# Performance work log

Measured on AMD Instinct MI355X. Metric: run time of the kernel, lower is better.

The kernel has to match this reference:

```python
import jax, jax.numpy as jnp
import numpy as np

WS = 8      # window size
SS = 4      # shift size
NH = 4      # num heads
EPS = 1e-5
MLP_RATIO = 4


def _win_part(x, ws):
    # x: [B,D,H,W,C] -> [B*nD*nH*nW, ws^3, C]
    B, D, H, W, C = x.shape
    x = x.reshape(B, D // ws, ws, H // ws, ws, W // ws, ws, C)
    x = x.transpose(0, 1, 3, 5, 2, 4, 6, 7)
    return x.reshape(-1, ws * ws * ws, C)


def _win_rev(w, ws, B, D, H, W):
    C = w.shape[-1]
    x = w.reshape(B, D // ws, H // ws, W // ws, ws, ws, ws, C)
    x = x.transpose(0, 1, 4, 2, 5, 3, 6, 7)
    return x.reshape(B, D, H, W, C)


def _ln(x, g, b):
    m = jnp.mean(x, axis=-1, keepdims=True)
    v = jnp.mean((x - m) ** 2, axis=-1, keepdims=True)
    return (x - m) / jnp.sqrt(v + EPS) * g + b


def _rel_index(ws):
    coords = np.stack(np.meshgrid(np.arange(ws), np.arange(ws), np.arange(ws), indexing='ij'))  # [3,ws,ws,ws]
    cf = coords.reshape(3, -1)                      # [3, ws^3]
    rel = (cf[:, :, None] - cf[:, None, :]).transpose(1, 2, 0) + (ws - 1)  # [N,N,3]
    return rel[..., 0] * (2 * ws - 1) ** 2 + rel[..., 1] * (2 * ws - 1) + rel[..., 2]


def _attn_mask(D, H, W, ws, ss):
    img = np.zeros((1, D, H, W, 1), dtype=np.float32)
    cnt = 0
    sl = (slice(0, -ws), slice(-ws, -ss), slice(-ss, None))
    for d in sl:
        for h in sl:
            for w in sl:
                img[:, d, h, w, :] = cnt
                cnt += 1
    mw = np.asarray(_win_part(jnp.asarray(img), ws))[..., 0]  # [nW, ws^3]
    diff = mw[:, None, :] - mw[:, :, None]
    return np.where(diff != 0, -100.0, 0.0).astype(np.float32)


def setup_inputs() -> dict:
    key = jax.random.key(0)
    ks = jax.random.split(key, 12)
    B, D, H, W, C = 1, 16, 64, 64, 128
    mh = MLP_RATIO * C
    s = 0.02
    return {
        'x': jax.random.normal(ks[0], (B, D, H, W, C), jnp.float32),
        'attn_mask': jnp.asarray(_attn_mask(D, H, W, WS, SS)),
        'rel_index': jnp.asarray(_rel_index(WS), jnp.int32),
        'rel_bias': jax.random.normal(ks[1], ((2 * WS - 1) ** 3, NH), jnp.float32) * s,
        'qkv_w': jax.random.normal(ks[2], (3 * C, C), jnp.float32) * s,
        'qkv_b': jnp.zeros((3 * C,), jnp.float32),
        'proj_w': jax.random.normal(ks[3], (C, C), jnp.float32) * s,
        'proj_b': jnp.zeros((C,), jnp.float32),
        'norm1_g': jnp.ones((C,), jnp.float32),
        'norm1_b': jnp.zeros((C,), jnp.float32),
        'norm2_g': jnp.ones((C,), jnp.float32),
        'norm2_b': jnp.zeros((C,), jnp.float32),
        'mlp_w1': jax.random.normal(ks[4], (mh, C), jnp.float32) * s,
        'mlp_b1': jnp.zeros((mh,), jnp.float32),
        'mlp_w2': jax.random.normal(ks[5], (C, mh), jnp.float32) * s,
        'mlp_b2': jnp.zeros((C,), jnp.float32),
    }


def reference(x, attn_mask, rel_index, rel_bias, qkv_w, qkv_b, proj_w, proj_b,
              norm1_g, norm1_b, norm2_g, norm2_b, mlp_w1, mlp_b1, mlp_w2, mlp_b2):
    B, D, H, W, C = x.shape
    ws, ss, nh = WS, SS, NH
    hd = C // nh
    scale = hd ** -0.5
    N = ws ** 3
    shortcut = x
    h = _ln(x, norm1_g, norm1_b)
    h = jnp.roll(h, (-ss, -ss, -ss), axis=(1, 2, 3))
    xw = _win_part(h, ws)                 # [B_, N, C]
    B_ = xw.shape[0]
    nW = attn_mask.shape[0]
    qkv = xw @ qkv_w.T + qkv_b            # [B_, N, 3C]
    qkv = qkv.reshape(B_, N, 3, nh, hd).transpose(2, 0, 3, 1, 4)  # [3,B_,h,N,hd]
    q, k, v = qkv[0] * scale, qkv[1], qkv[2]
    attn = jnp.einsum('bhnd,bhmd->bhnm', q, k)
    rpe = rel_bias[rel_index.reshape(-1)].reshape(N, N, nh).transpose(2, 0, 1)  # [h,N,N]
    attn = attn + rpe[None]
    attn = attn.reshape(B_ // nW, nW, nh, N, N) + attn_mask[None, :, None]
    attn = jax.nn.softmax(attn.reshape(B_, nh, N, N), axis=-1)
    out = jnp.einsum('bhnm,bhmd->bhnd', attn, v).transpose(0, 2, 1, 3).reshape(B_, N, C)
    out = out @ proj_w.T + proj_b
    out = _win_rev(out, ws, B, D, H, W)
    out = jnp.roll(out, (ss, ss, ss), axis=(1, 2, 3))
    x = shortcut + out
    h2 = _ln(x, norm2_g, norm2_b)
    h2 = jax.nn.gelu(h2 @ mlp_w1.T + mlp_b1, approximate=False)
    return x + h2 @ mlp_w2.T + mlp_b2
```

## Files before the change

kernel.cpp:

```cpp
#include <hip/hip_runtime.h>
#include <math.h>

typedef __bf16 bf16;
typedef __bf16 bf16x4 __attribute__((ext_vector_type(4)));
typedef __bf16 bf16x8 __attribute__((ext_vector_type(8)));
typedef float f32x4 __attribute__((ext_vector_type(4)));
typedef unsigned short u16;
typedef u16 u16x2 __attribute__((ext_vector_type(2)));

#define LOG2E 1.4426950408889634f

__device__ __forceinline__ float b2f(u16 b) {
  return (float)__builtin_bit_cast(bf16, b);
}

__global__ void sniff_k(const unsigned* __restrict__ xw_, int* __restrict__ flag) {
  int lane = threadIdx.x;
  int c = 0;
#pragma unroll
  for (int j = 0; j < 4; j++) {
    unsigned e = (xw_[lane * 4 + j] >> 7) & 0xFFu;
    c += (e >= 100u && e <= 140u) ? 1 : 0;
  }
#pragma unroll
  for (int d = 1; d < 64; d <<= 1) c += __shfl_xor(c, d);
  if (lane == 0) *flag = (c >= 150) ? 1 : 0;
}

struct ProArgs {
  const int* ridx;
  const void* rbias;
  bf16* rpem;
  const void* x;
  const bf16* g1;
  const bf16* b1n;
  bf16* xw;
  const void* csrc[12];
  bf16* cdst[12];
  int cn[12];
};

__global__ __launch_bounds__(256) void pro_k(ProArgs a,
                                             const int* __restrict__ flag) {
  const int bx = blockIdx.x, tid = threadIdx.x;
  const int fl = *flag;
  if (bx < 8192) {
    int t = bx * 256 + tid;
    int m0 = (t & 127) * 4, q = (t >> 7) & 511, h = (t >> 16) & 3, ty = t >> 18;
    int qd = q >> 6, qh = (q >> 3) & 7, qw = q & 7;
    int kt = m0 >> 6, mt = (m0 >> 4) & 3, quad = (m0 >> 2) & 3;
    int4 ri = *(const int4*)&a.ridx[q * 512 + m0];
    const int rv[4] = {ri.x, ri.y, ri.z, ri.w};
    bf16x4 o;
#pragma unroll
    for (int j = 0; j < 4; j++) {
      int m = m0 + j;
      int md = m >> 6, mh = (m >> 3) & 7, mw = m & 7;
      bool diff = ((ty & 4) && ((qd < 4) != (md < 4))) ||
                  ((ty & 2) && ((qh < 4) != (mh < 4))) ||
                  ((ty & 1) && ((qw < 4) != (mw < 4)));
      float bv = fl ? (float)((const bf16*)a.rbias)[rv[j] * 4 + h]
                    : ((const float*)a.rbias)[rv[j] * 4 + h];
      float v = bv * LOG2E;
      o[j] = (bf16)(v + (diff ? -144.2695041f : 0.f));
    }
    size_t out = ((size_t)(ty * 4 + h) << 18) +
                 (((size_t)(kt * 4 + quad) * 512 + q) * 16 + mt * 4);
    *(bf16x4*)&a.rpem[out] = o;
  } else if (bx < 24576) {
    int wave = tid >> 6, lane = tid & 63;
    int tok = (bx - 8192) * 4 + wave;
    int win = tok >> 9, pos = tok & 511;
    int rd = (win >> 6) * 8 + (pos >> 6);
    int rh = ((win >> 3) & 7) * 8 + ((pos >> 3) & 7);
    int rw = (win & 7) * 8 + (pos & 7);
    int od = (rd + 4) & 15, oh = (rh + 4) & 63, ow = (rw + 4) & 63;
    size_t src = (size_t)((od * 64 + oh) * 64 + ow) * 128;
    int ch = lane * 2;
    float f0, f1;
    if (!fl) {
      const float* xf = (const float*)a.x + src + ch;
      f0 = xf[0];
      f1 = xf[1];
    } else {
      u16x2 xv = *(const u16x2*)((const bf16*)a.x + src + ch);
      f0 = b2f(xv[0]);
      f1 = b2f(xv[1]);
    }
    float s = f0 + f1, sq = f0 * f0 + f1 * f1;
#pragma unroll
    for (int d = 1; d < 64; d <<= 1) {
      s += __shfl_xor(s, d);
      sq += __shfl_xor(sq, d);
    }
    float mean = s * (1.f / 128.f);
    float var = sq * (1.f / 128.f) - mean * mean;
    float rstd = rsqrtf(fmaxf(var, 0.f) + 1e-5f);
    u16x2 gv = *(const u16x2*)(a.g1 + ch), bv = *(const u16x2*)(a.b1n + ch);
    u16x2 ov;
    ov[0] =
        __builtin_bit_cast(u16, (bf16)((f0 - mean) * rstd * b2f(gv[0]) + b2f(bv[0])));
    ov[1] =
        __builtin_bit_cast(u16, (bf16)((f1 - mean) * rstd * b2f(gv[1]) + b2f(bv[1])));
    *(u16x2*)(a.xw + (size_t)tok * 128 + ch) = ov;
  } else {
    int seg = bx - 24576;
    int ti = seg >> 8;
    int i = (seg & 255) * 256 + tid;
    if (i < a.cn[ti]) {
      if (fl)
        a.cdst[ti][i] = ((const bf16*)a.csrc[ti])[i];
      else
        a.cdst[ti][i] = (bf16)((const float*)a.csrc[ti])[i];
    }
  }
}

__global__ __launch_bounds__(256) void ln_k(const bf16* __restrict__ x,
                                            const bf16* __restrict__ g,
                                            const bf16* __restrict__ bsh,
                                            bf16* __restrict__ out) {
  int wave = threadIdx.x >> 6, lane = threadIdx.x & 63;
  int tok = blockIdx.x * 4 + wave;
  size_t src = (size_t)tok * 128;
  int ch = lane * 2;
  u16x2 xv = *(const u16x2*)(x + src + ch);
  float f0 = b2f(xv[0]), f1 = b2f(xv[1]);
  float s = f0 + f1, sq = f0 * f0 + f1 * f1;
#pragma unroll
  for (int d = 1; d < 64; d <<= 1) {
    s += __shfl_xor(s, d);
    sq += __shfl_xor(sq, d);
  }
  float mean = s * (1.f / 128.f);
  float var = sq * (1.f / 128.f) - mean * mean;
  float rstd = rsqrtf(fmaxf(var, 0.f) + 1e-5f);
  u16x2 gv = *(const u16x2*)(g + ch), bv = *(const u16x2*)(bsh + ch);
  u16x2 ov;
  ov[0] = __builtin_bit_cast(u16, (bf16)((f0 - mean) * rstd * b2f(gv[0]) + b2f(bv[0])));
  ov[1] = __builtin_bit_cast(u16, (bf16)((f1 - mean) * rstd * b2f(gv[1]) + b2f(bv[1])));
  *(u16x2*)(out + (size_t)tok * 128 + ch) = ov;
}

template <int EPI, int BM, int BK, int N_, int K_>
__global__ __launch_bounds__(256) void gemm_k(const bf16* __restrict__ A,
                                              const bf16* __restrict__ B,
                                              const bf16* __restrict__ bias,
                                              void* __restrict__ outv,
                                              const void* __restrict__ residv,
                                              const int* __restrict__ flag) {
  constexpr int NC = K_ / BK;
  constexpr int NBUF = (NC > 1) ? 2 : 1;
  __shared__ __align__(16) u16 SM[NBUF][(BM + 128) * BK];
  const int t = threadIdx.x;
  const int wave = t >> 6, lane = t & 63, l15 = lane & 15, quad = lane >> 4;
  const int m0 = blockIdx.x * BM, n0 = blockIdx.y * 128;
  constexpr int MI = BM / 32;
  int fl = 0;
  if constexpr (EPI == 1) fl = *flag;
  f32x4 acc[MI][4] = {};
  const int wr = (wave >> 1) * (BM / 2), wc = (wave & 1) * 64;
  constexpr int TPR = BK / 8;
  constexpr int RPP = 256 / TPR;
  constexpr int PASSES = (BM + 128) / RPP;
  const int srow = t / TPR, sc16 = t % TPR;

  auto stage = [&](int c, int buf) {
#pragma unroll
    for (int p = 0; p < PASSES; p++) {
      int row = p * RPP + srow;
      int cs = sc16 ^ (row & 7);
      const u16* src;
      if (row < BM)
        src = (const u16*)A + (size_t)(m0 + row) * K_ + c * BK + cs * 8;
      else
        src = (const u16*)B + (size_t)(n0 + row - BM) * K_ + c * BK + cs * 8;
      __builtin_amdgcn_global_load_lds(
          (const __attribute__((address_space(1))) void*)src,
          (__attribute__((address_space(3))) void*)&SM[buf][row * BK + sc16 * 8],
          16, 0, 0);
    }
  };

  stage(0, 0);
  __syncthreads();
#pragma unroll
  for (int c = 0; c < NC; c++) {
    if (c + 1 < NC) stage(c + 1, (c + 1) & 1);
    const char* cur = (const char*)SM[c & 1];
#pragma unroll
    for (int ks = 0; ks < BK / 32; ks++) {
      bf16x8 a[MI], b[4];
#pragma unroll
      for (int i = 0; i < MI; i++) {
        int row = wr + i * 16 + l15;
        a[i] = *(const bf16x8*)(cur + row * (BK * 2) +
                                (((ks * 4 + quad) ^ (row & 7)) << 4));
      }
#pragma unroll
      for (int j = 0; j < 4; j++) {
        int row = BM + wc + j * 16 + l15;
        b[j] = *(const bf16x8*)(cur + row * (BK * 2) +
                                (((ks * 4 + quad) ^ (row & 7)) << 4));
      }
#pragma unroll
      for (int i = 0; i < MI; i++)
#pragma unroll
        for (int j = 0; j < 4; j++)
          acc[i][j] =
              __builtin_amdgcn_mfma_f32_16x16x32_bf16(a[i], b[j], acc[i][j], 0, 0, 0);
    }
    if (c + 1 < NC) __syncthreads();
  }
  const float qscale = 0.17677669529663687f * LOG2E;
#pragma unroll
  for (int i = 0; i < MI; i++) {
#pragma unroll
    for (int r = 0; r < 4; r++) {
      int tok = m0 + wr + i * 16 + quad * 4 + r;
      size_t obase = 0;
      if constexpr (EPI == 1) {
        int win = tok >> 9, pos = tok & 511;
        int rd = (win >> 6) * 8 + (pos >> 6);
        int rh = ((win >> 3) & 7) * 8 + ((pos >> 3) & 7);
        int rw = (win & 7) * 8 + (pos & 7);
        int od = (rd + 4) & 15, oh = (rh + 4) & 63, ow = (rw + 4) & 63;
        obase = (size_t)((od * 64 + oh) * 64 + ow) * 128;
      }
#pragma unroll
      for (int j = 0; j < 4; j++) {
        int gn = n0 + wc + j * 16 + l15;
        float v = acc[i][j][r] + (float)bias[gn];
        if constexpr (EPI == 0) {
          int tensor = gn >> 7, c = gn & 127, head = c >> 5, d = c & 31;
          if (tensor == 0) v *= qscale;
          int win = tok >> 9, pos = tok & 511;
          size_t off = ((((size_t)tensor * 4 + head) * 128 + win) * 512 + pos) * 32 + d;
          ((bf16*)outv)[off] = (bf16)v;
        } else {
          float rs = fl ? (float)((const bf16*)residv)[obase + gn]
                        : ((const float*)residv)[obase + gn];
          v += rs;
          ((bf16*)outv)[obase + gn] = (bf16)v;
        }
      }
    }
  }
}

__global__ __launch_bounds__(256) void mlp_k(const bf16* __restrict__ A,
                                             const bf16* __restrict__ W1,
                                             const bf16* __restrict__ B1,
                                             const bf16* __restrict__ W2,
                                             const bf16* __restrict__ B2,
                                             const bf16* __restrict__ resid,
                                             void* __restrict__ outv,
                                             const int* __restrict__ flag) {
  __shared__ __align__(16) u16 sA[32 * 128];
  __shared__ __align__(16) u16 sB[128 * 128];
  __shared__ __align__(16) u16 sH[32 * 520];
  const int t = threadIdx.x;
  const int wave = t >> 6, lane = t & 63, l15 = lane & 15, quad = lane >> 4;
  const int m0 = blockIdx.x * 32;
  const int wr = (wave >> 1) * 16, wc = (wave & 1) * 64;
  const int fl = *flag;
  const int srow = t >> 4, sc16 = t & 15;

  auto stage_w = [&](const bf16* W, int chunk, int wK) {
#pragma unroll
    for (int p = 0; p < 8; p++) {
      int row = p * 16 + srow;
      int cs = sc16 ^ (row & 7);
      const u16* src = (const u16*)W + (size_t)(wK == 128 ? (chunk * 128 + row) : row) *
                                           wK +
                       (wK == 128 ? 0 : chunk * 128) + cs * 8;
      __builtin_amdgcn_global_load_lds(
          (const __attribute__((address_space(1))) void*)src,
          (__attribute__((address_space(3))) void*)&sB[row * 128 + sc16 * 8], 16,
          0, 0);
    }
  };

  {
#pragma unroll
    for (int p = 0; p < 2; p++) {
      int row = p * 16 + srow;
      int cs = sc16 ^ (row & 7);
      __builtin_amdgcn_global_load_lds(
          (const __attribute__((address_space(1))) void*)((const u16*)A +
                                                          (size_t)(m0 + row) * 128 +
                                                          cs * 8),
          (__attribute__((address_space(3))) void*)&sA[row * 128 + sc16 * 8], 16,
          0, 0);
    }
  }
  stage_w(W1, 0, 128);
  __syncthreads();

#pragma unroll 1
  for (int nc = 0; nc < 4; nc++) {
    f32x4 acc1[4] = {};
#pragma unroll
    for (int ks = 0; ks < 4; ks++) {
      int arow = wr + l15;
      bf16x8 av = *(const bf16x8*)((const char*)sA + arow * 256 +
                                   (((ks * 4 + quad) ^ (arow & 7)) << 4));
      bf16x8 bv[4];
#pragma unroll
      for (int j = 0; j < 4; j++) {
        int row = wc + j * 16 + l15;
        bv[j] = *(const bf16x8*)((const char*)sB + row * 256 +
                                 (((ks * 4 + quad) ^ (row & 7)) << 4));
      }
#pragma unroll
      for (int j = 0; j < 4; j++)
        acc1[j] = __builtin_amdgcn_mfma_f32_16x16x32_bf16(av, bv[j], acc1[j], 0, 0, 0);
    }
#pragma unroll
    for (int j = 0; j < 4; j++) {
      int ncol = nc * 128 + wc + j * 16 + l15;
      float bj = (float)B1[ncol];
#pragma unroll
      for (int r = 0; r < 4; r++) {
        float v = acc1[j][r] + bj;
        float v2 = v * v;
        float u2 = v * (2.30220806f + 0.10294323f * v2);
        float e2 = exp2f(u2);
        v = v - v * __builtin_amdgcn_rcpf(e2 + 1.f);
        sH[(wr + quad * 4 + r) * 520 + ncol] = __builtin_bit_cast(u16, (bf16)v);
      }
    }
    __syncthreads();
    if (nc < 3)
      stage_w(W1, nc + 1, 128);
    else
      stage_w(W2, 0, 512);
    __syncthreads();
  }

  f32x4 acc2[4] = {};
#pragma unroll 1
  for (int kc = 0; kc < 4; kc++) {
#pragma unroll
    for (int ks = 0; ks < 4; ks++) {
      int arow = wr + l15;
      bf16x8 av = *(const bf16x8*)((const char*)sH + arow * 1040 +
                                   (kc * 128 + ks * 32 + quad * 8) * 2);
      bf16x8 bv[4];
#pragma unroll
      for (int j = 0; j < 4; j++) {
        int row = wc + j * 16 + l15;
        bv[j] = *(const bf16x8*)((const char*)sB + row * 256 +
                                 (((ks * 4 + quad) ^ (row & 7)) << 4));
      }
#pragma unroll
      for (int j = 0; j < 4; j++)
        acc2[j] = __builtin_amdgcn_mfma_f32_16x16x32_bf16(av, bv[j], acc2[j], 0, 0, 0);
    }
    if (kc < 3) {
      __syncthreads();
      stage_w(W2, kc + 1, 512);
      __syncthreads();
    }
  }
#pragma unroll
  for (int j = 0; j < 4; j++) {
    int gn = wc + j * 16 + l15;
    float bj = (float)B2[gn];
#pragma unroll
    for (int r = 0; r < 4; r++) {
      int tok = m0 + wr + quad * 4 + r;
      size_t off = (size_t)tok * 128 + gn;
      float v = acc2[j][r] + bj + (float)resid[off];
      if (fl)
        ((bf16*)outv)[off] = (bf16)v;
      else
        ((float*)outv)[off] = v;
    }
  }
}

__global__ __launch_bounds__(512, 4) void attn_k(const bf16* __restrict__ qkv,
                                                 const bf16* __restrict__ rpem,
                                                 bf16* __restrict__ att) {
  __shared__ __align__(16) bf16 sVt[32 * 512];
  __shared__ __align__(16) bf16 sP[8][32 * 64];
  const int t = threadIdx.x;
  const int p = blockIdx.x;
  const int win = ((p >> 6) << 3) | (p & 7);
  const int mid = (p >> 3) & 7;
  const int head = mid >> 1, qh = mid & 1;
  const int wave = t >> 6, lane = t & 63, l15 = lane & 15, quad = lane >> 4;

  const int wd = win >> 6, wh = (win >> 3) & 7, ww = win & 7;
  const int type = ((wd == 1) << 2) | ((wh == 7) << 1) | (ww == 7);

  const size_t hw32 = (size_t)512 * 32;
  const bf16* qp = qkv + ((size_t)(0 * 4 + head) * 128 + win) * hw32;
  const bf16* kp = qkv + ((size_t)(1 * 4 + head) * 128 + win) * hw32;
  const bf16* vp = qkv + ((size_t)(2 * 4 + head) * 128 + win) * hw32;
  const bf16* rpeh = rpem + ((size_t)(type * 4 + head) << 18);
  const int qbase = qh * 256 + wave * 32;

  {
    int kpi = t >> 3, dblk = (t & 7) * 4;
    char* sb = (char*)sVt;
#pragma unroll
    for (int kb = 0; kb < 4; kb++) {
      const bf16* v0 = vp + (size_t)(kb * 128 + 2 * kpi) * 32 + dblk;
      bf16x4 a = *(const bf16x4*)v0;
      bf16x4 b = *(const bf16x4*)(v0 + 32);
      int keyw = kb * 64 + kpi;
#pragma unroll
      for (int dd = 0; dd < 4; dd++) {
        int row = dblk + dd;
        unsigned wv = (unsigned)__builtin_bit_cast(u16, a[dd]) |
                      ((unsigned)__builtin_bit_cast(u16, b[dd]) << 16);
        *(unsigned*)(sb + ((row * 1024 + keyw * 4) ^ ((row & 7) << 4))) = wv;
      }
    }
  }

  bf16x8 qa[2];
#pragma unroll
  for (int nt = 0; nt < 2; nt++)
    qa[nt] = *(const bf16x8*)(qp + (size_t)(qbase + nt * 16 + l15) * 32 + quad * 8);

  bf16x8 ones;
#pragma unroll
  for (int e = 0; e < 8; e++) ones[e] = (bf16)1.0f;

  __syncthreads();

  f32x4 O[2][2] = {};
  f32x4 O2[2] = {};
  char* pw = (char*)sP[wave];
  const char* sv = (const char*)sVt;
  const int swz = (l15 & 7) << 4;

#pragma unroll 1
  for (int kt = 0; kt < 8; kt++) {
    bf16x8 kb[4];
    bf16x8 rv8[2][2];
#pragma unroll
    for (int mt = 0; mt < 4; mt++)
      kb[mt] = *(const bf16x8*)(kp + (size_t)(kt * 64 + mt * 16 + l15) * 32 +
                                quad * 8);
#pragma unroll
    for (int nt = 0; nt < 2; nt++) {
      const bf16* rb =
          rpeh + ((size_t)(kt * 4 + quad) * 512 + (qbase + nt * 16 + l15)) * 16;
      rv8[nt][0] = *(const bf16x8*)rb;
      rv8[nt][1] = *(const bf16x8*)(rb + 8);
    }
    f32x4 S[4][2];
#pragma unroll
    for (int mt = 0; mt < 4; mt++)
#pragma unroll
      for (int nt = 0; nt < 2; nt++) {
        f32x4 c;
#pragma unroll
        for (int r = 0; r < 4; r++) c[r] = (float)rv8[nt][mt >> 1][(mt & 1) * 4 + r];
        S[mt][nt] = __builtin_amdgcn_mfma_f32_16x16x32_bf16(kb[mt], qa[nt], c, 0, 0, 0);
      }
#pragma unroll
    for (int nt = 0; nt < 2; nt++)
#pragma unroll
      for (int mt = 0; mt < 4; mt++) {
        bf16x4 pv;
#pragma unroll
        for (int r = 0; r < 4; r++) pv[r] = (bf16)exp2f(S[mt][nt][r]);
        *(bf16x4*)(pw + (((nt * 16 + l15) * 128 + mt * 32 + quad * 8) ^ swz)) = pv;
      }
#pragma unroll
    for (int s = 0; s < 2; s++) {
      int vc = kt * 128 + s * 64 + quad * 16;
      int pc = s * 64 + quad * 16;
      bf16x8 va0 = *(const bf16x8*)(sv + ((l15 * 1024 + vc) ^ swz));
      bf16x8 va1 = *(const bf16x8*)(sv + (((16 + l15) * 1024 + vc) ^ swz));
      bf16x8 pb0 = *(const bf16x8*)(pw + ((l15 * 128 + pc) ^ swz));
      bf16x8 pb1 = *(const bf16x8*)(pw + (((16 + l15) * 128 + pc) ^ swz));
      O[0][0] = __builtin_amdgcn_mfma_f32_16x16x32_bf16(va0, pb0, O[0][0], 0, 0, 0);
      O[0][1] = __builtin_amdgcn_mfma_f32_16x16x32_bf16(va0, pb1, O[0][1], 0, 0, 0);
      O[1][0] = __builtin_amdgcn_mfma_f32_16x16x32_bf16(va1, pb0, O[1][0], 0, 0, 0);
      O[1][1] = __builtin_amdgcn_mfma_f32_16x16x32_bf16(va1, pb1, O[1][1], 0, 0, 0);
      O2[0] = __builtin_amdgcn_mfma_f32_16x16x32_bf16(ones, pb0, O2[0], 0, 0, 0);
      O2[1] = __builtin_amdgcn_mfma_f32_16x16x32_bf16(ones, pb1, O2[1], 0, 0, 0);
    }
  }
#pragma unroll
  for (int nt = 0; nt < 2; nt++) {
    float inv = __builtin_amdgcn_rcpf(O2[nt][0]);
    int q = qbase + nt * 16 + l15;
#pragma unroll
    for (int dm = 0; dm < 2; dm++) {
      bf16x4 o;
#pragma unroll
      for (int r = 0; r < 4; r++) o[r] = (bf16)(O[dm][nt][r] * inv);
      *(bf16x4*)(att + ((size_t)win * 512 + q) * 128 + head * 32 + dm * 16 +
                 quad * 4) = o;
    }
  }
}

extern "C" void kernel_launch(void* const* d_in, const int* in_sizes, int n_in,
                              void* d_out, int out_size, void* d_ws,
                              size_t ws_size, hipStream_t stream) {
  const int* rel_index = (const int*)d_in[2];
  char* w = (char*)d_ws;

  int* flag = (int*)w;
  bf16* qw_c = (bf16*)(w + (128ull << 10));
  bf16* pw_c = (bf16*)(w + (256ull << 10));
  bf16* w1_c = (bf16*)(w + (320ull << 10));
  bf16* w2_c = (bf16*)(w + (512ull << 10));
  bf16* qb_c = (bf16*)(w + (704ull << 10));
  bf16* pb_c = (bf16*)(w + (708ull << 10));
  bf16* g1_c = (bf16*)(w + (712ull << 10));
  bf16* b1n_c = (bf16*)(w + (716ull << 10));
  bf16* g2_c = (bf16*)(w + (720ull << 10));
  bf16* b2n_c = (bf16*)(w + (724ull << 10));
  bf16* mb1_c = (bf16*)(w + (728ull << 10));
  bf16* mb2_c = (bf16*)(w + (732ull << 10));
  bf16* xw = (bf16*)(w + (17ull << 20));
  bf16* qkvb = (bf16*)(w + (33ull << 20));
  bf16* x2 = (bf16*)(w + (99ull << 20));
  bf16* rpem = x2;
  bf16* att = xw;
  bf16* h2 = xw;

  sniff_k<<<1, 64, 0, stream>>>((const unsigned*)d_in[0], flag);

  ProArgs pa;
  pa.ridx = rel_index;
  pa.rbias = d_in[3];
  pa.rpem = rpem;
  pa.x = d_in[0];
  pa.g1 = g1_c;
  pa.b1n = b1n_c;
  pa.xw = xw;
  const int srcidx[12] = {4, 5, 6, 7, 8, 9, 10, 11, 12, 13, 14, 15};
  bf16* dsts[12] = {qw_c, qb_c, pw_c, pb_c, g1_c, b1n_c,
                    g2_c, b2n_c, w1_c, mb1_c, w2_c, mb2_c};
  for (int i = 0; i < 12; i++) {
    pa.csrc[i] = d_in[srcidx[i]];
    pa.cdst[i] = dsts[i];
    pa.cn[i] = in_sizes[srcidx[i]];
  }
  {
    CanonFix:;
  }
  struct NormFixArgs {
    const void* s[4];
    bf16* d[4];
  };
  auto canon_norm = [&]() {};
  (void)canon_norm;
  {
    struct MiniArgs {
      const void* src[2];
      bf16* dst[2];
      int n[2];
    };
    static_assert(sizeof(MiniArgs) <= 64, "");
  }
  {
    ProArgs dummy = pa;
    (void)dummy;
  }
  {
  }
  extern __global__ void canon_norm_k(const void*, const void*, bf16*, bf16*,
                                      const int*);
  canon_norm_k<<<1, 256, 0, stream>>>(d_in[8], d_in[9], g1_c, b1n_c, flag);

  pro_k<<<27648, 256, 0, stream>>>(pa, flag);
  gemm_k<0, 32, 128, 384, 128><<<dim3(2048, 3), 256, 0, stream>>>(
      xw, qw_c, qb_c, qkvb, nullptr, flag);
  attn_k<<<1024, 512, 0, stream>>>(qkvb, rpem, att);
  gemm_k<1, 32, 128, 128, 128><<<dim3(2048, 1), 256, 0, stream>>>(
      att, pw_c, pb_c, x2, d_in[0], flag);
  ln_k<<<16384, 256, 0, stream>>>(x2, g2_c, b2n_c, h2);
  mlp_k<<<2048, 256, 0, stream>>>(h2, w1_c, mb1_c, w2_c, mb2_c, x2, d_out, flag);
}

__global__ __launch_bounds__(256) void canon_norm_k(
    const void* __restrict__ sg, const void* __restrict__ sb,
    bf16* __restrict__ dg, bf16* __restrict__ db, const int* __restrict__ flag) {
  int i = threadIdx.x;
  int fl = *flag;
  if (i < 128) {
    dg[i] = fl ? ((const bf16*)sg)[i] : (bf16)((const float*)sg)[i];
  } else {
    int j = i - 128;
    db[j] = fl ? ((const bf16*)sb)[j] : (bf16)((const float*)sb)[j];
  }
}
```

Baseline: 384.9 us.

## Double-buffer MLP weight tiles and pass attention probabilities via lane shuffles

The MLP kernel now stages weights in two half-size LDS buffers and prefetches the next chunk while the current one feeds the MFMAs. This removes one barrier per chunk and hides global-to-LDS latency behind compute. The attention kernel no longer writes exp'd scores to a per-wave LDS scratch; it rearranges them into the PV operand layout with cross-lane shuffles, which frees LDS and raises the occupancy hint from 4 to 6 blocks. The shuffle path adds VALU work and register pressure, and the smaller MLP tiles issue more, smaller MFMA groups. canon_norm_k is moved ahead of the host code and the dead scaffolding is removed.

```diff
diff --git a/kernel.cpp b/kernel.cpp
--- a/kernel.cpp
+++ b/kernel.cpp
@@ -5,6 +5,7 @@
 typedef __bf16 bf16x4 __attribute__((ext_vector_type(4)));
 typedef __bf16 bf16x8 __attribute__((ext_vector_type(8)));
 typedef float f32x4 __attribute__((ext_vector_type(4)));
+typedef unsigned u32x4 __attribute__((ext_vector_type(4)));
 typedef unsigned short u16;
 typedef u16 u16x2 __attribute__((ext_vector_type(2)));
 
@@ -25,6 +26,19 @@
 #pragma unroll
   for (int d = 1; d < 64; d <<= 1) c += __shfl_xor(c, d);
   if (lane == 0) *flag = (c >= 150) ? 1 : 0;
+}
+
+__global__ __launch_bounds__(256) void canon_norm_k(
+    const void* __restrict__ sg, const void* __restrict__ sb,
+    bf16* __restrict__ dg, bf16* __restrict__ db, const int* __restrict__ flag) {
+  int i = threadIdx.x;
+  int fl = *flag;
+  if (i < 128) {
+    dg[i] = fl ? ((const bf16*)sg)[i] : (bf16)((const float*)sg)[i];
+  } else {
+    int j = i - 128;
+    db[j] = fl ? ((const bf16*)sb)[j] : (bf16)((const float*)sb)[j];
+  }
 }
 
 struct ProArgs {
@@ -257,31 +271,46 @@
                                              void* __restrict__ outv,
                                              const int* __restrict__ flag) {
   __shared__ __align__(16) u16 sA[32 * 128];
-  __shared__ __align__(16) u16 sB[128 * 128];
+  __shared__ __align__(16) u16 sB[2][64 * 128];
   __shared__ __align__(16) u16 sH[32 * 520];
   const int t = threadIdx.x;
   const int wave = t >> 6, lane = t & 63, l15 = lane & 15, quad = lane >> 4;
   const int m0 = blockIdx.x * 32;
-  const int wr = (wave >> 1) * 16, wc = (wave & 1) * 64;
+  const int wr = (wave >> 1) * 16;
   const int fl = *flag;
-  const int srow = t >> 4, sc16 = t & 15;
-
-  auto stage_w = [&](const bf16* W, int chunk, int wK) {
-#pragma unroll
-    for (int p = 0; p < 8; p++) {
+
+  auto stage_w1 = [&](int chunk, int buf) {
+    int srow = t >> 4, sc16 = t & 15;
+#pragma unroll
+    for (int p = 0; p < 4; p++) {
       int row = p * 16 + srow;
       int cs = sc16 ^ (row & 7);
-      const u16* src = (const u16*)W + (size_t)(wK == 128 ? (chunk * 128 + row) : row) *
-                                           wK +
-                       (wK == 128 ? 0 : chunk * 128) + cs * 8;
       __builtin_amdgcn_global_load_lds(
-          (const __attribute__((address_space(1))) void*)src,
-          (__attribute__((address_space(3))) void*)&sB[row * 128 + sc16 * 8], 16,
-          0, 0);
+          (const __attribute__((address_space(1))) void*)((const u16*)W1 +
+                                                          (size_t)(chunk * 64 + row) *
+                                                              128 +
+                                                          cs * 8),
+          (__attribute__((address_space(3))) void*)&sB[buf][row * 128 + sc16 * 8],
+          16, 0, 0);
     }
   };
+  auto stage_w2 = [&](int chunk, int buf) {
+    int srow = t >> 3, sc8 = t & 7;
+#pragma unroll
+    for (int p = 0; p < 4; p++) {
+      int row = p * 32 + srow;
+      int cs = sc8 ^ (row & 7);
+      __builtin_amdgcn_global_load_lds(
+          (const __attribute__((address_space(1))) void*)((const u16*)W2 +
+                                                          (size_t)row * 512 +
+                                                          chunk * 64 + cs * 8),
+          (__attribute__((address_space(3))) void*)&sB[buf][row * 64 + sc8 * 8],
+          16, 0, 0);
+    }
+  };
 
   {
+    int srow = t >> 4, sc16 = t & 15;
 #pragma unroll
     for (int p = 0; p < 2; p++) {
       int row = p * 16 + srow;
@@ -294,31 +323,30 @@
           0, 0);
     }
   }
-  stage_w(W1, 0, 128);
+  stage_w1(0, 0);
   __syncthreads();
 
 #pragma unroll 1
-  for (int nc = 0; nc < 4; nc++) {
-    f32x4 acc1[4] = {};
+  for (int nc = 0; nc < 8; nc++) {
+    if (nc < 7) stage_w1(nc + 1, (nc + 1) & 1);
+    const char* bs = (const char*)sB[nc & 1];
+    f32x4 acc1[2] = {};
 #pragma unroll
     for (int ks = 0; ks < 4; ks++) {
       int arow = wr + l15;
       bf16x8 av = *(const bf16x8*)((const char*)sA + arow * 256 +
                                    (((ks * 4 + quad) ^ (arow & 7)) << 4));
-      bf16x8 bv[4];
-#pragma unroll
-      for (int j = 0; j < 4; j++) {
-        int row = wc + j * 16 + l15;
-        bv[j] = *(const bf16x8*)((const char*)sB + row * 256 +
-                                 (((ks * 4 + quad) ^ (row & 7)) << 4));
-      }
-#pragma unroll
-      for (int j = 0; j < 4; j++)
-        acc1[j] = __builtin_amdgcn_mfma_f32_16x16x32_bf16(av, bv[j], acc1[j], 0, 0, 0);
-    }
-#pragma unroll
-    for (int j = 0; j < 4; j++) {
-      int ncol = nc * 128 + wc + j * 16 + l15;
+#pragma unroll
+      for (int j = 0; j < 2; j++) {
+        int row = (wave & 1) * 32 + j * 16 + l15;
+        bf16x8 bv = *(const bf16x8*)(bs + row * 256 +
+                                     (((ks * 4 + quad) ^ (row & 7)) << 4));
+        acc1[j] = __builtin_amdgcn_mfma_f32_16x16x32_bf16(av, bv, acc1[j], 0, 0, 0);
+      }
+    }
+#pragma unroll
+    for (int j = 0; j < 2; j++) {
+      int ncol = nc * 64 + (wave & 1) * 32 + j * 16 + l15;
       float bj = (float)B1[ncol];
 #pragma unroll
       for (int r = 0; r < 4; r++) {
@@ -331,41 +359,33 @@
       }
     }
     __syncthreads();
-    if (nc < 3)
-      stage_w(W1, nc + 1, 128);
-    else
-      stage_w(W2, 0, 512);
-    __syncthreads();
-  }
+  }
+  stage_w2(0, 0);
+  __syncthreads();
 
   f32x4 acc2[4] = {};
 #pragma unroll 1
-  for (int kc = 0; kc < 4; kc++) {
-#pragma unroll
-    for (int ks = 0; ks < 4; ks++) {
+  for (int kc = 0; kc < 8; kc++) {
+    if (kc < 7) stage_w2(kc + 1, (kc + 1) & 1);
+    const char* bs = (const char*)sB[kc & 1];
+#pragma unroll
+    for (int ks = 0; ks < 2; ks++) {
       int arow = wr + l15;
       bf16x8 av = *(const bf16x8*)((const char*)sH + arow * 1040 +
-                                   (kc * 128 + ks * 32 + quad * 8) * 2);
-      bf16x8 bv[4];
+                                   (kc * 64 + ks * 32 + quad * 8) * 2);
 #pragma unroll
       for (int j = 0; j < 4; j++) {
-        int row = wc + j * 16 + l15;
-        bv[j] = *(const bf16x8*)((const char*)sB + row * 256 +
-                                 (((ks * 4 + quad) ^ (row & 7)) << 4));
-      }
-#pragma unroll
-      for (int j = 0; j < 4; j++)
-        acc2[j] = __builtin_amdgcn_mfma_f32_16x16x32_bf16(av, bv[j], acc2[j], 0, 0, 0);
-    }
-    if (kc < 3) {
-      __syncthreads();
-      stage_w(W2, kc + 1, 512);
-      __syncthreads();
-    }
+        int row = (wave & 1) * 64 + j * 16 + l15;
+        bf16x8 bv = *(const bf16x8*)(bs + row * 128 +
+                                     (((ks * 4 + quad) ^ (row & 7)) << 4));
+        acc2[j] = __builtin_amdgcn_mfma_f32_16x16x32_bf16(av, bv, acc2[j], 0, 0, 0);
+      }
+    }
+    if (kc < 7) __syncthreads();
   }
 #pragma unroll
   for (int j = 0; j < 4; j++) {
-    int gn = wc + j * 16 + l15;
+    int gn = (wave & 1) * 64 + j * 16 + l15;
     float bj = (float)B2[gn];
 #pragma unroll
     for (int r = 0; r < 4; r++) {
@@ -380,11 +400,10 @@
   }
 }
 
-__global__ __launch_bounds__(512, 4) void attn_k(const bf16* __restrict__ qkv,
+__global__ __launch_bounds__(512, 6) void attn_k(const bf16* __restrict__ qkv,
                                                  const bf16* __restrict__ rpem,
                                                  bf16* __restrict__ att) {
   __shared__ __align__(16) bf16 sVt[32 * 512];
-  __shared__ __align__(16) bf16 sP[8][32 * 64];
   const int t = threadIdx.x;
   const int p = blockIdx.x;
   const int win = ((p >> 6) << 3) | (p & 7);
@@ -434,9 +453,10 @@
 
   f32x4 O[2][2] = {};
   f32x4 O2[2] = {};
-  char* pw = (char*)sP[wave];
   const char* sv = (const char*)sVt;
   const int swz = (l15 & 7) << 4;
+  const int srcA = (quad & 1) * 32 + l15;
+  const bool hiMt = (quad >> 1) != 0;
 
 #pragma unroll 1
   for (int kt = 0; kt < 8; kt++) {
@@ -453,39 +473,53 @@
       rv8[nt][0] = *(const bf16x8*)rb;
       rv8[nt][1] = *(const bf16x8*)(rb + 8);
     }
-    f32x4 S[4][2];
-#pragma unroll
-    for (int mt = 0; mt < 4; mt++)
+#pragma unroll
+    for (int s = 0; s < 2; s++) {
+      unsigned pk[2][2][2];
+#pragma unroll
+      for (int ml = 0; ml < 2; ml++) {
+        const int mt = 2 * s + ml;
+#pragma unroll
+        for (int nt = 0; nt < 2; nt++) {
+          f32x4 c;
+#pragma unroll
+          for (int r = 0; r < 4; r++)
+            c[r] = (float)rv8[nt][mt >> 1][(mt & 1) * 4 + r];
+          f32x4 Sv =
+              __builtin_amdgcn_mfma_f32_16x16x32_bf16(kb[mt], qa[nt], c, 0, 0, 0);
+          u16 h0 = __builtin_bit_cast(u16, (bf16)exp2f(Sv[0]));
+          u16 h1 = __builtin_bit_cast(u16, (bf16)exp2f(Sv[1]));
+          u16 h2 = __builtin_bit_cast(u16, (bf16)exp2f(Sv[2]));
+          u16 h3 = __builtin_bit_cast(u16, (bf16)exp2f(Sv[3]));
+          pk[ml][nt][0] = (unsigned)h0 | ((unsigned)h1 << 16);
+          pk[ml][nt][1] = (unsigned)h2 | ((unsigned)h3 << 16);
+        }
+      }
+      bf16x8 pb[2];
 #pragma unroll
       for (int nt = 0; nt < 2; nt++) {
-        f32x4 c;
-#pragma unroll
-        for (int r = 0; r < 4; r++) c[r] = (float)rv8[nt][mt >> 1][(mt & 1) * 4 + r];
-        S[mt][nt] = __builtin_amdgcn_mfma_f32_16x16x32_bf16(kb[mt], qa[nt], c, 0, 0, 0);
-      }
-#pragma unroll
-    for (int nt = 0; nt < 2; nt++)
-#pragma unroll
-      for (int mt = 0; mt < 4; mt++) {
-        bf16x4 pv;
-#pragma unroll
-        for (int r = 0; r < 4; r++) pv[r] = (bf16)exp2f(S[mt][nt][r]);
-        *(bf16x4*)(pw + (((nt * 16 + l15) * 128 + mt * 32 + quad * 8) ^ swz)) = pv;
-      }
-#pragma unroll
-    for (int s = 0; s < 2; s++) {
+        u32x4 uv;
+#pragma unroll
+        for (int half = 0; half < 2; half++) {
+          int srcl = srcA + half * 16;
+#pragma unroll
+          for (int wq = 0; wq < 2; wq++) {
+            unsigned x0 = (unsigned)__shfl((int)pk[0][nt][wq], srcl);
+            unsigned x1 = (unsigned)__shfl((int)pk[1][nt][wq], srcl);
+            uv[half * 2 + wq] = hiMt ? x1 : x0;
+          }
+        }
+        pb[nt] = __builtin_bit_cast(bf16x8, uv);
+      }
       int vc = kt * 128 + s * 64 + quad * 16;
-      int pc = s * 64 + quad * 16;
       bf16x8 va0 = *(const bf16x8*)(sv + ((l15 * 1024 + vc) ^ swz));
       bf16x8 va1 = *(const bf16x8*)(sv + (((16 + l15) * 1024 + vc) ^ swz));
-      bf16x8 pb0 = *(const bf16x8*)(pw + ((l15 * 128 + pc) ^ swz));
-      bf16x8 pb1 = *(const bf16x8*)(pw + (((16 + l15) * 128 + pc) ^ swz));
-      O[0][0] = __builtin_amdgcn_mfma_f32_16x16x32_bf16(va0, pb0, O[0][0], 0, 0, 0);
-      O[0][1] = __builtin_amdgcn_mfma_f32_16x16x32_bf16(va0, pb1, O[0][1], 0, 0, 0);
-      O[1][0] = __builtin_amdgcn_mfma_f32_16x16x32_bf16(va1, pb0, O[1][0], 0, 0, 0);
-      O[1][1] = __builtin_amdgcn_mfma_f32_16x16x32_bf16(va1, pb1, O[1][1], 0, 0, 0);
-      O2[0] = __builtin_amdgcn_mfma_f32_16x16x32_bf16(ones, pb0, O2[0], 0, 0, 0);
-      O2[1] = __builtin_amdgcn_mfma_f32_16x16x32_bf16(ones, pb1, O2[1], 0, 0, 0);
+      O[0][0] = __builtin_amdgcn_mfma_f32_16x16x32_bf16(va0, pb[0], O[0][0], 0, 0, 0);
+      O[0][1] = __builtin_amdgcn_mfma_f32_16x16x32_bf16(va0, pb[1], O[0][1], 0, 0, 0);
+      O[1][0] = __builtin_amdgcn_mfma_f32_16x16x32_bf16(va1, pb[0], O[1][0], 0, 0, 0);
+      O[1][1] = __builtin_amdgcn_mfma_f32_16x16x32_bf16(va1, pb[1], O[1][1], 0, 0, 0);
+      O2[0] = __builtin_amdgcn_mfma_f32_16x16x32_bf16(ones, pb[0], O2[0], 0, 0, 0);
+      O2[1] = __builtin_amdgcn_mfma_f32_16x16x32_bf16(ones, pb[1], O2[1], 0, 0, 0);
     }
   }
 #pragma unroll
@@ -530,6 +564,7 @@
   bf16* h2 = xw;
 
   sniff_k<<<1, 64, 0, stream>>>((const unsigned*)d_in[0], flag);
+  canon_norm_k<<<1, 256, 0, stream>>>(d_in[8], d_in[9], g1_c, b1n_c, flag);
 
   ProArgs pa;
   pa.ridx = rel_index;
@@ -547,34 +582,8 @@
     pa.cdst[i] = dsts[i];
     pa.cn[i] = in_sizes[srcidx[i]];
   }
-  {
-    CanonFix:;
-  }
-  struct NormFixArgs {
-    const void* s[4];
-    bf16* d[4];
-  };
-  auto canon_norm = [&]() {};
-  (void)canon_norm;
-  {
-    struct MiniArgs {
-      const void* src[2];
-      bf16* dst[2];
-      int n[2];
-    };
-    static_assert(sizeof(MiniArgs) <= 64, "");
-  }
-  {
-    ProArgs dummy = pa;
-    (void)dummy;
-  }
-  {
-  }
-  extern __global__ void canon_norm_k(const void*, const void*, bf16*, bf16*,
-                                      const int*);
-  canon_norm_k<<<1, 256, 0, stream>>>(d_in[8], d_in[9], g1_c, b1n_c, flag);
-
   pro_k<<<27648, 256, 0, stream>>>(pa, flag);
+
   gemm_k<0, 32, 128, 384, 128><<<dim3(2048, 3), 256, 0, stream>>>(
       xw, qw_c, qb_c, qkvb, nullptr, flag);
   attn_k<<<1024, 512, 0, stream>>>(qkvb, rpem, att);
@@ -583,16 +592,3 @@
   ln_k<<<16384, 256, 0, stream>>>(x2, g2_c, b2n_c, h2);
   mlp_k<<<2048, 256, 0, stream>>>(h2, w1_c, mb1_c, w2_c, mb2_c, x2, d_out, flag);
 }
-
-__global__ __launch_bounds__(256) void canon_norm_k(
-    const void* __restrict__ sg, const void* __restrict__ sb,
-    bf16* __restrict__ dg, bf16* __restrict__ db, const int* __restrict__ flag) {
-  int i = threadIdx.x;
-  int fl = *flag;
-  if (i < 128) {
-    dg[i] = fl ? ((const bf16*)sg)[i] : (bf16)((const float*)sg)[i];
-  } else {
-    int j = i - 128;
-    db[j] = fl ? ((const bf16*)sb)[j] : (bf16)((const float*)sb)[j];
-  }
-}
```

After: 413.7 us. +7.5%, slower.
